# Kernel tuning notes

Hardware: AMD Instinct MI355X
Metric: run time of the kernel (lower is better)

The kernel has to match this reference:

```python
import jax, jax.numpy as jnp
from jax import lax
import numpy as np

B, M, C, H, W = 32, 2, 256, 16, 16
N = H * W            # 256, square case required by the original bmm chain
DIM = 256            # hardcoded self.dim in the module
THR = 0.1
RATIO = 0.8


def conv2d(x, w, b):
    y = lax.conv_general_dilated(x, w, (1, 1), 'SAME',
                                 dimension_numbers=('NCHW', 'OIHW', 'NCHW'))
    return y + b[None, :, None, None]


def setup_inputs() -> dict:
    key = jax.random.key(0)
    ks = jax.random.split(key, 8)
    return {
        'con_feat': jax.random.normal(ks[0], (B, M, C, H, W), jnp.float32),
        'feat_s':   jax.random.normal(ks[1], (B, M, C, C), jnp.float32),
        'feat_v':   jax.random.uniform(ks[2], (B, M, C), jnp.float32),
        'feat_d':   jax.random.normal(ks[3], (B, M, N, N), jnp.float32),
        'w_enc':    jax.random.normal(ks[4], (C, C, 3, 3), jnp.float32) * 0.02,
        'b_enc':    jnp.zeros((C,), jnp.float32),
        'w_dec':    jax.random.normal(ks[5], (C, C, 3, 3), jnp.float32) * 0.02,
        'b_dec':    jnp.zeros((C,), jnp.float32),
        'w_val':    jax.random.normal(ks[6], (1, 2 * C, 3, 3), jnp.float32) * 0.02,
        'b_val':    jnp.zeros((1,), jnp.float32),
    }


def _assemble(fs, fv, fd, counts):
    # fs: (M,C,C) row blocks, fv: (M,C) diag values, fd: (M,N,N) col blocks, counts: (M,)
    big = max(C, N)                                  # out-of-range sentinel -> dropped
    off = jnp.cumsum(counts) - counts                # exclusive prefix offsets (M,)
    r = jnp.arange(C)
    dest = off[:, None] + r[None, :]                 # (M,C) destination slots
    valid = (r[None, :] < counts[:, None]) & (dest >= 0)
    dest = jnp.where(valid, dest, big).reshape(-1)   # (M*C,)
    ns = jnp.zeros((C, C), fs.dtype).at[dest].set(fs.reshape(M * C, C), mode='drop')
    fd_cols = fd[:, :, :C].transpose(0, 2, 1).reshape(M * C, N)  # source columns as rows
    ndT = jnp.zeros((N, N), fd.dtype).at[dest].set(fd_cols, mode='drop')
    nv = jnp.zeros((C, N), fv.dtype).at[dest, dest].set(fv.reshape(-1), mode='drop')
    return ns, nv, ndT.T


def reference(con_feat, feat_s, feat_v, feat_d, w_enc, b_enc, w_dec, b_dec, w_val, b_val):
    x = con_feat.reshape(B * M, C, H, W)
    # autoencoder reconstruction loss (training branch)
    mid = jax.nn.relu(conv2d(x, w_enc, b_enc))
    x_rec = conv2d(mid, w_dec, b_dec)
    auto_enc_loss = jnp.mean((x - x_rec) ** 2)

    # data-dependent rank budget per (batch, modality)
    counts = jnp.sum(feat_v > THR, axis=-1).astype(jnp.int32)      # (B,M)
    total = jnp.sum(counts, axis=-1)                               # (B,)
    kmin = min(C, N)
    adj = jnp.round(kmin * counts.astype(jnp.float32)
                    / jnp.maximum(total, 1)[:, None].astype(jnp.float32)).astype(jnp.int32)
    if M > 1:
        adj = adj.at[:, -1].set(DIM - jnp.sum(adj[:, :-1], axis=-1))
    counts = jnp.maximum(jnp.where((total > kmin)[:, None], adj, counts), 0)

    # scatter-assemble s/v/d and reconstruct
    ns, nv, nd = jax.vmap(_assemble)(feat_s, feat_v, feat_d, counts)
    rec = jnp.matmul(jnp.matmul(ns, nv), nd)                        # (B,C,N)
    rec = rec.reshape(B, C, H, W)
    rec = conv2d(rec, w_dec, b_dec)                                 # decoder
    rec = (rec - rec.min()) / (rec.max() - rec.min()) * 2.0 - 1.0

    # per-modality value scores, softmax over modality
    scores = jnp.stack([
        jax.nn.sigmoid(jax.nn.relu(conv2d(
            jnp.concatenate([rec, con_feat[:, m]], axis=1), w_val, b_val)))
        for m in range(M)
    ], axis=1)                                                      # (B,M,1,H,W)
    scores = jax.nn.softmax(scores, axis=1)
    fused = jnp.sum((1.0 - RATIO) * scores * con_feat, axis=1) + rec * RATIO
    return fused, auto_enc_loss
```

## Files before the change

### kernel.cpp

```cpp
#include <hip/hip_runtime.h>
#include <math.h>


typedef __attribute__((ext_vector_type(8))) short short8;
typedef __attribute__((ext_vector_type(4))) float f32x4;

__device__ __forceinline__ void gload_lds16(const void* g, void* l) {
  __builtin_amdgcn_global_load_lds(
      (const __attribute__((address_space(1))) void*)g,
      (__attribute__((address_space(3))) void*)l, 16, 0, 0);
}

__device__ __forceinline__ unsigned short f2bf(float f) {
  unsigned u = __float_as_uint(f);
  unsigned r = (u + 0x7FFFu + ((u >> 16) & 1u)) >> 16;
  return (unsigned short)r;
}

__device__ __forceinline__ unsigned mapf(float f) {
  unsigned u = __float_as_uint(f);
  return (u & 0x80000000u) ? ~u : (u | 0x80000000u);
}
__device__ __forceinline__ float unmapf(unsigned u) {
  unsigned v = (u & 0x80000000u) ? (u & 0x7fffffffu) : ~u;
  return __uint_as_float(v);
}

__global__ __launch_bounds__(256) void prep_k(
    const float* __restrict__ cf, const float* __restrict__ we,
    const float* __restrict__ wd, const float* __restrict__ fv,
    unsigned short* __restrict__ Xp, unsigned short* __restrict__ WrE,
    unsigned short* __restrict__ WrD, int* __restrict__ smr,
    float* __restrict__ vd, float4* __restrict__ sraw4,
    float* __restrict__ lacc, unsigned* __restrict__ mm) {
  const int bx = blockIdx.x, t = threadIdx.x;
  if (bx < 2048) {
    int xcdP = bx >> 8, r = bx & 255;
    int img = xcdP * 8 + (r >> 5), ch = r & 31;
    int p = t;
    int ic0 = ch * 8;
    const float* sp = cf + (size_t)img * 65536 + (size_t)ic0 * 256 + p;
    unsigned short h[8];
#pragma unroll
    for (int i = 0; i < 8; ++i) h[i] = f2bf(sp[i * 256]);
    int y = p >> 4, x = p & 15;
    uint4 u;
    u.x = h[0] | (h[1] << 16); u.y = h[2] | (h[3] << 16);
    u.z = h[4] | (h[5] << 16); u.w = h[6] | (h[7] << 16);
    *(uint4*)&Xp[(size_t)img * 82944 + (size_t)(y * 18 + x + 19) * 256 + ic0] = u;
  } else if (bx < 2624) {
    int idx = (bx - 2048) * 256 + t;
    int ch = idx & 31, rest = idx >> 5;
    int s = rest % 9, ocx = rest / 9;
    int oc = ocx & 255, cv = ocx >> 8;
    const float* w = cv ? wd : we;
    unsigned short* o = cv ? WrD : WrE;
    int ic0 = ch * 8;
    unsigned short h[8];
#pragma unroll
    for (int i = 0; i < 8; ++i) h[i] = f2bf(w[(size_t)oc * 2304 + (ic0 + i) * 9 + s]);
    uint4 u;
    u.x = h[0] | (h[1] << 16); u.y = h[2] | (h[3] << 16);
    u.z = h[4] | (h[5] << 16); u.w = h[6] | (h[7] << 16);
    *(uint4*)&o[(size_t)oc * 2304 + s * 256 + ic0] = u;
  } else if (bx < 2752) {
    int img = bx - 2624;
    uint4* base = (uint4*)Xp + (size_t)img * 10368;
    uint4 z; z.x = z.y = z.z = z.w = 0;
    for (int it = t; it < 2176; it += 256) {
      int px = it >> 5, c = it & 31;
      int y, x;
      if (px < 18)      { y = 0;  x = px; }
      else if (px < 36) { y = 17; x = px - 18; }
      else if (px < 52) { y = px - 35; x = 0; }
      else              { y = px - 51; x = 17; }
      base[(y * 18 + x) * 32 + c] = z;
    }
  } else if (bx < 2784) {
    const int b = bx - 2752;
    const float v0 = fv[(size_t)b * 512 + t];
    const float v1 = fv[(size_t)b * 512 + 256 + t];
    const unsigned long long bal0 = __ballot(v0 > 0.1f);
    const unsigned long long bal1 = __ballot(v1 > 0.1f);
    __shared__ int cnt0[4], cnt1[4], fc[2];
    const int wid = t >> 6, lane = t & 63;
    if (lane == 0) { cnt0[wid] = __popcll(bal0); cnt1[wid] = __popcll(bal1); }
    smr[b * 256 + t] = -1;
    vd[b * 256 + t] = 0.f;
    __syncthreads();
    if (t == 0) {
      int c0 = cnt0[0] + cnt0[1] + cnt0[2] + cnt0[3];
      int c1 = cnt1[0] + cnt1[1] + cnt1[2] + cnt1[3];
      int total = c0 + c1;
      int f0, f1;
      if (total > 256) {
        int a0 = (int)rintf(256.0f * (float)c0 / (float)total);
        f0 = a0; f1 = 256 - a0;
      } else { f0 = c0; f1 = c1; }
      fc[0] = max(f0, 0); fc[1] = max(f1, 0);
    }
    __syncthreads();
    const int c0 = fc[0], c1 = fc[1];
    if (t < c0) { smr[b * 256 + t] = t; vd[b * 256 + t] = v0; }
    if (t < c1) {
      int d = c0 + t;
      if (d < 256) { smr[b * 256 + d] = 256 + t; vd[b * 256 + d] = v1; }
    }
  } else {
    int z = bx - 2784;
    if (z < 24) {
      float4 zz; zz.x = zz.y = zz.z = zz.w = 0.f;
      sraw4[z * 256 + t] = zz;
    } else if (t == 0) {
      lacc[0] = 0.f; mm[0] = 0xFFFFFFFFu; mm[1] = 0u;
    }
  }
}

__global__ __launch_bounds__(256) void ansbmt_k(
    const float* __restrict__ fs, const float* __restrict__ fd,
    const int* __restrict__ smr, const float* __restrict__ vd,
    unsigned short* __restrict__ Ans, unsigned short* __restrict__ BmT,
    unsigned short* __restrict__ Recp) {
  const int bx = blockIdx.x, t = threadIdx.x;
  if (bx < 1024) {
    int idx = bx * 256 + t;
    int ch = idx & 31, c = (idx >> 5) & 255, b = idx >> 13;
    int j0 = ch * 8;
    int si = smr[b * 256 + c];
    unsigned short h[8] = {0, 0, 0, 0, 0, 0, 0, 0};
    if (si >= 0) {
      int m = si >> 8, r = si & 255;
      const float* fp = fs + (((size_t)b * 2 + m) * 256 + r) * 256 + j0;
      const float* vp = vd + b * 256 + j0;
#pragma unroll
      for (int i = 0; i < 8; ++i) h[i] = f2bf(fp[i] * vp[i]);
    }
    uint4 u;
    u.x = h[0] | (h[1] << 16); u.y = h[2] | (h[3] << 16);
    u.z = h[4] | (h[5] << 16); u.w = h[6] | (h[7] << 16);
    *(uint4*)&Ans[(size_t)b * 65536 + c * 256 + j0] = u;
  } else if (bx < 2048) {
    __shared__ float sIn[4096];
    const int q0 = bx - 1024;
    const int b = q0 >> 5, jg = q0 & 31;
    const int sp = smr[b * 256 + t];
    const int m_p = sp >> 8, r_p = sp & 255;
#pragma unroll
    for (int u = 0; u < 4; ++u) {
      int q = t * 4 + u;
      int rr = q >> 6, w = q & 63;
      int m = rr >> 3, i = rr & 7;
      float4 f = ((const float4*)fd)[((size_t)(b * 2 + m) * 256 + jg * 8 + i) * 64 + w];
      *(float4*)&sIn[i * 512 + m * 256 + w * 4] = f;
    }
    __syncthreads();
    unsigned short h[8] = {0, 0, 0, 0, 0, 0, 0, 0};
    if (sp >= 0) {
#pragma unroll
      for (int i = 0; i < 8; ++i) h[i] = f2bf(sIn[i * 512 + m_p * 256 + r_p]);
    }
    uint4 u;
    u.x = h[0] | (h[1] << 16); u.y = h[2] | (h[3] << 16);
    u.z = h[4] | (h[5] << 16); u.w = h[6] | (h[7] << 16);
    *(uint4*)&BmT[(size_t)b * 65536 + t * 256 + jg * 8] = u;
  } else {
    int img = bx - 2048;
    uint4* base = (uint4*)Recp + (size_t)img * 10368;
    uint4 z; z.x = z.y = z.z = z.w = 0;
    for (int it = t; it < 2176; it += 256) {
      int px = it >> 5, c = it & 31;
      int y, x;
      if (px < 18)      { y = 0;  x = px; }
      else if (px < 36) { y = 17; x = px - 18; }
      else if (px < 52) { y = px - 35; x = 0; }
      else              { y = px - 51; x = 17; }
      base[(y * 18 + x) * 32 + c] = z;
    }
  }
}

__global__ __launch_bounds__(256, 3) void encrec_k(
    const unsigned short* __restrict__ Xin, const unsigned short* __restrict__ Wr,
    const float* __restrict__ bias,          unsigned short* __restrict__ outp,
    const unsigned short* __restrict__ BmT,  const unsigned short* __restrict__ Ans,
    unsigned short* __restrict__ Recp) {
  __shared__ __align__(16) char SS[49152];
  const int t = threadIdx.x, lane = t & 63, wave = t >> 6;
  const int L = blockIdx.x;

  if (L < 512) {
    char (*S)[24576] = (char(*)[24576])SS;
    const int xcd = L & 7, sl = L >> 3;
    const int img = xcd * 8 + (sl & 7);
    const int tile = sl >> 3;
    const int pt = tile & 3, ot = tile >> 2;

    int laneA[2], laneB[4];
#pragma unroll
    for (int r = 0; r < 2; ++r) {
      int id = r * 256 + t;
      int row = id >> 3, sub = id & 7, q = sub ^ (row & 7);
      int p = pt * 64 + row, y = p >> 4, x = p & 15;
      laneA[r] = (y * 18 + x) * 512 + q * 16;
    }
#pragma unroll
    for (int r = 0; r < 4; ++r) {
      int id = r * 256 + t;
      int row = id >> 3, sub = id & 7, q = sub ^ (row & 7);
      laneB[r] = (ot * 128 + row) * 4608 + q * 16;
    }
    const char* Ag = (const char*)Xin + (size_t)img * 165888;
    const char* Bg = (const char*)Wr;

    const int mlane = lane & 15, quad = lane >> 4;
    const int mw = wave >> 1, nw = wave & 1;
    int aoff[2][2], boff[4][2];
#pragma unroll
    for (int ks = 0; ks < 2; ++ks) {
#pragma unroll
      for (int i = 0; i < 2; ++i) {
        int rowm = mw * 32 + i * 16 + mlane;
        aoff[i][ks] = rowm * 128 + (((ks * 4 + quad) ^ (rowm & 7)) * 16);
      }
#pragma unroll
      for (int n = 0; n < 4; ++n) {
        int rown = nw * 64 + n * 16 + mlane;
        boff[n][ks] = 8192 + rown * 128 + (((ks * 4 + quad) ^ (rown & 7)) * 16);
      }
    }

    auto stage = [&](int kit, int buf) {
      int s = kit >> 2;
      int dy = s / 3, dx = s - dy * 3;
      int aG = (dy * 18 + dx) * 512 + (kit & 3) * 128;
      int bG = kit * 128;
      char* dst = S[buf];
#pragma unroll
      for (int r = 0; r < 2; ++r)
        gload_lds16(Ag + laneA[r] + aG, dst + r * 4096 + wave * 1024);
#pragma unroll
      for (int r = 0; r < 4; ++r)
        gload_lds16(Bg + laneB[r] + bG, dst + 8192 + r * 4096 + wave * 1024);
    };

    f32x4 acc[2][4] = {};
    auto compute = [&](int buf) {
      const char* Sb = S[buf];
#pragma unroll
      for (int ks = 0; ks < 2; ++ks) {
        short8 af[2], bf[4];
#pragma unroll
        for (int i = 0; i < 2; ++i) af[i] = *(const short8*)(Sb + aoff[i][ks]);
#pragma unroll
        for (int n = 0; n < 4; ++n) bf[n] = *(const short8*)(Sb + boff[n][ks]);
#pragma unroll
        for (int i = 0; i < 2; ++i)
#pragma unroll
          for (int n = 0; n < 4; ++n)
            acc[i][n] = __builtin_amdgcn_mfma_f32_16x16x32_bf16(af[i], bf[n], acc[i][n], 0, 0, 0);
      }
    };

    stage(0, 0);
    for (int kit = 0; kit < 36; ++kit) {
      int cur = kit & 1;
      asm volatile("s_waitcnt vmcnt(0)" ::: "memory");
      asm volatile("s_barrier" ::: "memory");
      if (kit + 1 < 36) stage(kit + 1, 1 - cur);
      compute(cur);
    }

#pragma unroll
    for (int i = 0; i < 2; ++i) {
      int m0 = pt * 64 + mw * 32 + i * 16 + quad * 4;
#pragma unroll
      for (int n = 0; n < 4; ++n) {
        int oc = ot * 128 + nw * 64 + n * 16 + mlane;
        float bv = bias[oc];
#pragma unroll
        for (int r = 0; r < 4; ++r) {
          int p = m0 + r;
          int y = p >> 4, x = p & 15;
          float v = fmaxf(acc[i][n][r] + bv, 0.f);
          outp[(size_t)img * 82944 + (size_t)(y * 18 + x + 19) * 256 + oc] = f2bf(v);
        }
      }
    }
  } else {
    unsigned short (*S)[8192] = (unsigned short(*)[8192])SS;
    const int L2 = L - 512;
    const int b = L2 >> 4, tile = L2 & 15;
    const int pt = tile >> 2, ct = tile & 3;

    int laneA[2], laneB[2];
#pragma unroll
    for (int j = 0; j < 2; ++j) {
      int id = (wave * 2 + j) * 64 + lane;
      int row = id >> 3, q = (id & 7) ^ (row & 7);
      laneA[j] = (pt * 64 + row) * 512 + q * 16;
      laneB[j] = (ct * 64 + row) * 512 + q * 16;
    }
    const char* Ag = (const char*)BmT + (size_t)b * 131072;
    const char* Bg = (const char*)Ans + (size_t)b * 131072;

    const int mlane = lane & 15, quad = lane >> 4;
    const int mw = wave >> 1, nw = wave & 1;
    int aoff[2][2], boff[2][2];
#pragma unroll
    for (int ks = 0; ks < 2; ++ks) {
#pragma unroll
      for (int i = 0; i < 2; ++i) {
        int rowm = mw * 32 + i * 16 + mlane;
        aoff[i][ks] = rowm * 128 + (((ks * 4 + quad) ^ (rowm & 7)) * 16);
        int rown = nw * 32 + i * 16 + mlane;
        boff[i][ks] = 8192 + rown * 128 + (((ks * 4 + quad) ^ (rown & 7)) * 16);
      }
    }

    auto stage = [&](int kit, int buf) {
      int g = kit * 128;
      char* dst = (char*)S[buf];
#pragma unroll
      for (int j = 0; j < 2; ++j)
        gload_lds16(Ag + laneA[j] + g, dst + (wave * 2 + j) * 1024);
#pragma unroll
      for (int j = 0; j < 2; ++j)
        gload_lds16(Bg + laneB[j] + g, dst + 8192 + (wave * 2 + j) * 1024);
    };

    f32x4 acc[2][2] = {};
    auto compute = [&](int buf) {
      const char* Sb = (const char*)S[buf];
#pragma unroll
      for (int ks = 0; ks < 2; ++ks) {
        short8 af[2], bf[2];
#pragma unroll
        for (int i = 0; i < 2; ++i) {
          af[i] = *(const short8*)(Sb + aoff[i][ks]);
          bf[i] = *(const short8*)(Sb + boff[i][ks]);
        }
#pragma unroll
        for (int i = 0; i < 2; ++i)
#pragma unroll
          for (int n = 0; n < 2; ++n)
            acc[i][n] = __builtin_amdgcn_mfma_f32_16x16x32_bf16(af[i], bf[n], acc[i][n], 0, 0, 0);
      }
    };

    stage(0, 0);
    stage(1, 1);
    for (int kit = 0; kit < 3; ++kit) {
      asm volatile("s_waitcnt vmcnt(4)" ::: "memory");
      asm volatile("s_barrier" ::: "memory");
      int nb = kit + 2;
      if (nb < 4) stage(nb, nb % 3);
      compute(kit % 3);
    }
    asm volatile("s_waitcnt vmcnt(0)" ::: "memory");
    asm volatile("s_barrier" ::: "memory");
    compute(3 % 3);

#pragma unroll
    for (int i = 0; i < 2; ++i) {
      int m0 = pt * 64 + mw * 32 + i * 16 + quad * 4;
#pragma unroll
      for (int n = 0; n < 2; ++n) {
        int cc = ct * 64 + nw * 32 + n * 16 + mlane;
#pragma unroll
        for (int r = 0; r < 4; ++r) {
          int p = m0 + r;
          int y = p >> 4, x = p & 15;
          Recp[(size_t)b * 82944 + (size_t)(y * 18 + x + 19) * 256 + cc] = f2bf(acc[i][n][r]);
        }
      }
    }
  }
}

__global__ __launch_bounds__(256, 3) void conv_dec_k(
    const unsigned short* __restrict__ Midp, const unsigned short* __restrict__ Recp,
    const unsigned short* __restrict__ Wr, const float* __restrict__ bias,
    const float* __restrict__ cfref, float* __restrict__ rec2,
    float* __restrict__ lacc, unsigned* __restrict__ mm) {
  __shared__ __align__(16) char S[2][24576];
  const int t = threadIdx.x, lane = t & 63, wave = t >> 6;
  const int L = blockIdx.x;
  const int xcd = L & 7, sl = L >> 3;
  const int u12 = sl % 12, tile = sl / 12;
  const bool isLoss = u12 < 8;
  const int unit = isLoss ? (xcd * 8 + u12) : (64 + xcd * 4 + (u12 - 8));
  const int pt = tile & 3, ot = tile >> 2;

  int laneA[2], laneB[4];
#pragma unroll
  for (int r = 0; r < 2; ++r) {
    int id = r * 256 + t;
    int row = id >> 3, sub = id & 7, q = sub ^ (row & 7);
    int p = pt * 64 + row, y = p >> 4, x = p & 15;
    laneA[r] = (y * 18 + x) * 512 + q * 16;
  }
#pragma unroll
  for (int r = 0; r < 4; ++r) {
    int id = r * 256 + t;
    int row = id >> 3, sub = id & 7, q = sub ^ (row & 7);
    laneB[r] = (ot * 128 + row) * 4608 + q * 16;
  }
  const char* Ag = isLoss ? (const char*)Midp + (size_t)unit * 165888
                          : (const char*)Recp + (size_t)(unit - 64) * 165888;
  const char* Bg = (const char*)Wr;

  const int mlane = lane & 15, quad = lane >> 4;
  const int mw = wave >> 1, nw = wave & 1;
  int aoff[2][2], boff[4][2];
#pragma unroll
  for (int ks = 0; ks < 2; ++ks) {
#pragma unroll
    for (int i = 0; i < 2; ++i) {
      int rowm = mw * 32 + i * 16 + mlane;
      aoff[i][ks] = rowm * 128 + (((ks * 4 + quad) ^ (rowm & 7)) * 16);
    }
#pragma unroll
    for (int n = 0; n < 4; ++n) {
      int rown = nw * 64 + n * 16 + mlane;
      boff[n][ks] = 8192 + rown * 128 + (((ks * 4 + quad) ^ (rown & 7)) * 16);
    }
  }

  auto stage = [&](int kit, int buf) {
    int s = kit >> 2;
    int dy = s / 3, dx = s - dy * 3;
    int aG = (dy * 18 + dx) * 512 + (kit & 3) * 128;
    int bG = kit * 128;
    char* dst = S[buf];
#pragma unroll
    for (int r = 0; r < 2; ++r)
      gload_lds16(Ag + laneA[r] + aG, dst + r * 4096 + wave * 1024);
#pragma unroll
    for (int r = 0; r < 4; ++r)
      gload_lds16(Bg + laneB[r] + bG, dst + 8192 + r * 4096 + wave * 1024);
  };

  f32x4 acc[2][4] = {};
  auto compute = [&](int buf) {
    const char* Sb = S[buf];
#pragma unroll
    for (int ks = 0; ks < 2; ++ks) {
      short8 af[2], bf[4];
#pragma unroll
      for (int i = 0; i < 2; ++i) af[i] = *(const short8*)(Sb + aoff[i][ks]);
#pragma unroll
      for (int n = 0; n < 4; ++n) bf[n] = *(const short8*)(Sb + boff[n][ks]);
#pragma unroll
      for (int i = 0; i < 2; ++i)
#pragma unroll
        for (int n = 0; n < 4; ++n)
          acc[i][n] = __builtin_amdgcn_mfma_f32_16x16x32_bf16(af[i], bf[n], acc[i][n], 0, 0, 0);
    }
  };

  stage(0, 0);
  for (int kit = 0; kit < 36; ++kit) {
    int cur = kit & 1;
    asm volatile("s_waitcnt vmcnt(0)" ::: "memory");
    asm volatile("s_barrier" ::: "memory");
    if (kit + 1 < 36) stage(kit + 1, 1 - cur);
    compute(cur);
  }

  if (isLoss) {
    float ls = 0.f;
#pragma unroll
    for (int i = 0; i < 2; ++i) {
      int m0 = pt * 64 + mw * 32 + i * 16 + quad * 4;
#pragma unroll
      for (int n = 0; n < 4; ++n) {
        int oc = ot * 128 + nw * 64 + n * 16 + mlane;
        float bv = bias[oc];
        float4 c4 = *(const float4*)(cfref + (size_t)unit * 65536 + (size_t)oc * 256 + m0);
        float d0 = acc[i][n][0] + bv - c4.x;
        float d1 = acc[i][n][1] + bv - c4.y;
        float d2 = acc[i][n][2] + bv - c4.z;
        float d3 = acc[i][n][3] + bv - c4.w;
        ls += d0 * d0 + d1 * d1 + d2 * d2 + d3 * d3;
      }
    }
#pragma unroll
    for (int off = 32; off; off >>= 1) ls += __shfl_down(ls, off);
    __shared__ float sred[4];
    if (lane == 0) sred[wave] = ls;
    __syncthreads();
    if (t == 0) {
      float s = sred[0] + sred[1] + sred[2] + sred[3];
      atomicAdd(lacc, s);
    }
  } else {
    const int img2 = unit - 64;
    float mn = INFINITY, mx = -INFINITY;
#pragma unroll
    for (int i = 0; i < 2; ++i) {
      int m0 = pt * 64 + mw * 32 + i * 16 + quad * 4;
#pragma unroll
      for (int n = 0; n < 4; ++n) {
        int oc = ot * 128 + nw * 64 + n * 16 + mlane;
        float bv = bias[oc];
        float4 v;
        v.x = acc[i][n][0] + bv; v.y = acc[i][n][1] + bv;
        v.z = acc[i][n][2] + bv; v.w = acc[i][n][3] + bv;
        mn = fminf(mn, fminf(fminf(v.x, v.y), fminf(v.z, v.w)));
        mx = fmaxf(mx, fmaxf(fmaxf(v.x, v.y), fmaxf(v.z, v.w)));
        *(float4*)(rec2 + (size_t)img2 * 65536 + (size_t)oc * 256 + m0) = v;
      }
    }
#pragma unroll
    for (int off = 32; off; off >>= 1) {
      mn = fminf(mn, __shfl_down(mn, off));
      mx = fmaxf(mx, __shfl_down(mx, off));
    }
    __shared__ float smn[4], smx[4];
    if (lane == 0) { smn[wave] = mn; smx[wave] = mx; }
    __syncthreads();
    if (t == 0) {
      float a = fminf(fminf(smn[0], smn[1]), fminf(smn[2], smn[3]));
      float b2 = fmaxf(fmaxf(smx[0], smx[1]), fmaxf(smx[2], smx[3]));
      atomicMin(&mm[0], mapf(a));
      atomicMax(&mm[1], mapf(b2));
    }
  }
}

__global__ __launch_bounds__(256) void score_conv_k(
    const float* __restrict__ rec2, const float* __restrict__ cf,
    const float* __restrict__ wval, const unsigned* __restrict__ mm,
    float* __restrict__ sraw) {
  const int b = blockIdx.x, phase = blockIdx.y, icc = blockIdx.z;
  const int t = threadIdx.x;
  const int row = t >> 4, col = t & 15;
  __shared__ float s_in[8 * 360];
  __shared__ float s_wv[72];
  for (int i = t; i < 8 * 360; i += 256) s_in[i] = 0.f;
  const float* src;
  float sc = 1.f, sh = 0.f;
  int wofs;
  if (phase == 0) {
    src = rec2 + (size_t)b * 65536;
    float mn = unmapf(mm[0]), mx = unmapf(mm[1]);
    sc = 2.f / (mx - mn);
    sh = -mn * sc - 1.f;
    wofs = 0;
  } else {
    src = cf + ((size_t)b * 2 + (phase - 1)) * 65536;
    wofs = 2304;
  }
  float acc = 0.f;
  for (int ic0 = icc * 32; ic0 < icc * 32 + 32; ic0 += 8) {
    __syncthreads();
#pragma unroll
    for (int i = 0; i < 8; ++i) {
      float v = src[(ic0 + i) * 256 + t];
      if (phase == 0) v = fmaf(v, sc, sh);
      s_in[i * 360 + (row + 1) * 20 + (col + 1)] = v;
    }
    if (t < 72) s_wv[t] = wval[wofs + ic0 * 9 + t];
    __syncthreads();
#pragma unroll
    for (int i = 0; i < 8; ++i)
#pragma unroll
      for (int ky = 0; ky < 3; ++ky)
#pragma unroll
        for (int kx = 0; kx < 3; ++kx)
          acc += s_in[i * 360 + (row + ky) * 20 + (col + kx)] * s_wv[i * 9 + ky * 3 + kx];
  }
  atomicAdd(&sraw[((size_t)b * 3 + phase) * 256 + t], acc);
}

__global__ __launch_bounds__(256) void fuse_k(
    const float* __restrict__ cf, const float* __restrict__ rec2,
    const float* __restrict__ sraw, const float* __restrict__ bval,
    const unsigned* __restrict__ mm, const float* __restrict__ lacc,
    float* __restrict__ outp) {
  const int e0 = (blockIdx.x * 256 + threadIdx.x) * 4;
  const int b = e0 >> 16;
  const int rest = e0 & 65535;
  const int pos = e0 & 255;
  const float mn = unmapf(mm[0]), mx = unmapf(mm[1]);
  const float sc = 2.f / (mx - mn), sh = -mn * sc - 1.f;
  const float4 srec = *(const float4*)&sraw[(size_t)b * 768 + pos];
  const float4 scA  = *(const float4*)&sraw[(size_t)b * 768 + 256 + pos];
  const float4 scB  = *(const float4*)&sraw[(size_t)b * 768 + 512 + pos];
  const float bv = bval[0];
  const float4 r4 = *(const float4*)&rec2[e0];
  const float4 f0 = *(const float4*)&cf[(size_t)b * 131072 + rest];
  const float4 f1 = *(const float4*)&cf[(size_t)b * 131072 + 65536 + rest];
  float4 o;
#pragma unroll
  for (int k = 0; k < 4; ++k) {
    float sr = ((const float*)&srec)[k];
    float a0 = ((const float*)&scA)[k];
    float a1 = ((const float*)&scB)[k];
    float z0 = fmaxf(sr + a0 + bv, 0.f);
    float z1 = fmaxf(sr + a1 + bv, 0.f);
    float s0 = 1.f / (1.f + expf(-z0));
    float s1 = 1.f / (1.f + expf(-z1));
    float w0 = 1.f / (1.f + expf(s1 - s0));
    float w1 = 1.f - w0;
    float rn = fmaf(((const float*)&r4)[k], sc, sh);
    float g0 = ((const float*)&f0)[k];
    float g1 = ((const float*)&f1)[k];
    ((float*)&o)[k] = 0.2f * (w0 * g0 + w1 * g1) + 0.8f * rn;
  }
  *(float4*)&outp[e0] = o;
  if (e0 == 0) outp[2097152] = lacc[0] * (1.f / 4194304.f);
}

extern "C" void kernel_launch(void* const* d_in, const int* in_sizes, int n_in,
                              void* d_out, int out_size, void* d_ws, size_t ws_size,
                              hipStream_t stream) {
  const float* cf    = (const float*)d_in[0];
  const float* fs    = (const float*)d_in[1];
  const float* fv    = (const float*)d_in[2];
  const float* fd    = (const float*)d_in[3];
  const float* w_enc = (const float*)d_in[4];
  const float* b_enc = (const float*)d_in[5];
  const float* w_dec = (const float*)d_in[6];
  const float* b_dec = (const float*)d_in[7];
  const float* w_val = (const float*)d_in[8];
  const float* b_val = (const float*)d_in[9];
  float* out = (float*)d_out;
  float* wsf = (float*)d_ws;

  unsigned short* Xp   = (unsigned short*)wsf;
  unsigned short* Midp = (unsigned short*)(wsf + 2654208);
  unsigned short* Recp = (unsigned short*)(wsf + 5308416);
  float* rec2 = wsf + 6635520;
  unsigned short* WrE = (unsigned short*)(wsf + 8732672);
  unsigned short* WrD = (unsigned short*)(wsf + 9027584);
  unsigned short* Ans = (unsigned short*)(wsf + 9322496);
  unsigned short* BmT = (unsigned short*)(wsf + 10371072);
  float* sraw = wsf + 11419648;
  float* vd   = wsf + 11444224;
  int*   smr  = (int*)(wsf + 11452416);
  float* lacc = wsf + 11460608;
  unsigned* mm = (unsigned*)(wsf + 11460609);

  prep_k<<<2809, 256, 0, stream>>>(cf, w_enc, w_dec, fv, Xp, WrE, WrD, smr, vd,
                                   (float4*)sraw, lacc, mm);
  ansbmt_k<<<2080, 256, 0, stream>>>(fs, fd, smr, vd, Ans, BmT, Recp);
  encrec_k<<<1024, 256, 0, stream>>>(Xp, WrE, b_enc, Midp, BmT, Ans, Recp);
  conv_dec_k<<<768, 256, 0, stream>>>(Midp, Recp, WrD, b_dec, cf, rec2, lacc, mm);
  score_conv_k<<<dim3(32, 3, 8), 256, 0, stream>>>(rec2, cf, w_val, mm, sraw);
  fuse_k<<<2048, 256, 0, stream>>>(cf, rec2, sraw, b_val, mm, lacc, out);
}
```

Before: 212.5 us.

## Merge prep and assemble kernels; store decoder output as bf16

Folds the ansbmt kernel into the prep kernel. Each assemble block now recomputes the per-batch modality counts from feat_v with ballots instead of reading smr/vd index tables, which removes one launch and the dependency between them. The decoder output rec2 is stored as bf16 rather than fp32, halving its write and the two later reads in score_conv and fuse. Score_conv also reads weights directly from global memory instead of staging them in LDS. The cost is redundant count computation per block and reduced precision on the reconstruction used in the output.

Measured after the change: 219.9 us. +3.5%, slower.

```diff
diff --git a/kernel.cpp b/kernel.cpp
--- a/kernel.cpp
+++ b/kernel.cpp
@@ -16,6 +16,9 @@
   unsigned r = (u + 0x7FFFu + ((u >> 16) & 1u)) >> 16;
   return (unsigned short)r;
 }
+__device__ __forceinline__ float bf2f(unsigned short h) {
+  return __uint_as_float(((unsigned)h) << 16);
+}
 
 __device__ __forceinline__ unsigned mapf(float f) {
   unsigned u = __float_as_uint(f);
@@ -26,13 +29,15 @@
   return __uint_as_float(v);
 }
 
-__global__ __launch_bounds__(256) void prep_k(
+__global__ __launch_bounds__(256) void prep2_k(
     const float* __restrict__ cf, const float* __restrict__ we,
     const float* __restrict__ wd, const float* __restrict__ fv,
+    const float* __restrict__ fs, const float* __restrict__ fd,
     unsigned short* __restrict__ Xp, unsigned short* __restrict__ WrE,
-    unsigned short* __restrict__ WrD, int* __restrict__ smr,
-    float* __restrict__ vd, float4* __restrict__ sraw4,
-    float* __restrict__ lacc, unsigned* __restrict__ mm) {
+    unsigned short* __restrict__ WrD, unsigned short* __restrict__ Ans,
+    unsigned short* __restrict__ BmT, unsigned short* __restrict__ Recp,
+    float4* __restrict__ sraw4, float* __restrict__ lacc,
+    unsigned* __restrict__ mm) {
   const int bx = blockIdx.x, t = threadIdx.x;
   if (bx < 2048) {
     int xcdP = bx >> 8, r = bx & 255;
@@ -76,75 +81,65 @@
       else              { y = px - 51; x = 17; }
       base[(y * 18 + x) * 32 + c] = z;
     }
-  } else if (bx < 2784) {
-    const int b = bx - 2752;
+  } else if (bx < 3776) {
+    const int abx = bx - 2752;
+    const int b = abx >> 5;
     const float v0 = fv[(size_t)b * 512 + t];
     const float v1 = fv[(size_t)b * 512 + 256 + t];
     const unsigned long long bal0 = __ballot(v0 > 0.1f);
     const unsigned long long bal1 = __ballot(v1 > 0.1f);
-    __shared__ int cnt0[4], cnt1[4], fc[2];
-    const int wid = t >> 6, lane = t & 63;
-    if (lane == 0) { cnt0[wid] = __popcll(bal0); cnt1[wid] = __popcll(bal1); }
-    smr[b * 256 + t] = -1;
-    vd[b * 256 + t] = 0.f;
+    __shared__ int c0a[4], c1a[4];
+    if ((t & 63) == 0) { c0a[t >> 6] = __popcll(bal0); c1a[t >> 6] = __popcll(bal1); }
     __syncthreads();
-    if (t == 0) {
-      int c0 = cnt0[0] + cnt0[1] + cnt0[2] + cnt0[3];
-      int c1 = cnt1[0] + cnt1[1] + cnt1[2] + cnt1[3];
-      int total = c0 + c1;
-      int f0, f1;
-      if (total > 256) {
-        int a0 = (int)rintf(256.0f * (float)c0 / (float)total);
-        f0 = a0; f1 = 256 - a0;
-      } else { f0 = c0; f1 = c1; }
-      fc[0] = max(f0, 0); fc[1] = max(f1, 0);
-    }
-    __syncthreads();
-    const int c0 = fc[0], c1 = fc[1];
-    if (t < c0) { smr[b * 256 + t] = t; vd[b * 256 + t] = v0; }
-    if (t < c1) {
-      int d = c0 + t;
-      if (d < 256) { smr[b * 256 + d] = 256 + t; vd[b * 256 + d] = v1; }
-    }
-  } else {
-    int z = bx - 2784;
-    if (z < 24) {
-      float4 zz; zz.x = zz.y = zz.z = zz.w = 0.f;
-      sraw4[z * 256 + t] = zz;
-    } else if (t == 0) {
-      lacc[0] = 0.f; mm[0] = 0xFFFFFFFFu; mm[1] = 0u;
-    }
-  }
-}
-
-__global__ __launch_bounds__(256) void ansbmt_k(
-    const float* __restrict__ fs, const float* __restrict__ fd,
-    const int* __restrict__ smr, const float* __restrict__ vd,
-    unsigned short* __restrict__ Ans, unsigned short* __restrict__ BmT,
-    unsigned short* __restrict__ Recp) {
-  const int bx = blockIdx.x, t = threadIdx.x;
-  if (bx < 1024) {
-    int idx = bx * 256 + t;
-    int ch = idx & 31, c = (idx >> 5) & 255, b = idx >> 13;
+    int c0 = c0a[0] + c0a[1] + c0a[2] + c0a[3];
+    int c1 = c1a[0] + c1a[1] + c1a[2] + c1a[3];
+    int total = c0 + c1, f0, f1;
+    if (total > 256) {
+      int a0 = (int)rintf(256.0f * (float)c0 / (float)total);
+      f0 = a0; f1 = 256 - a0;
+    } else { f0 = c0; f1 = c1; }
+    f0 = max(f0, 0); f1 = max(f1, 0);
+
+    int idx = abx * 256 + t;
+    int ch = idx & 31, c = (idx >> 5) & 255;
     int j0 = ch * 8;
-    int si = smr[b * 256 + c];
+    int si = (c < f0) ? c : ((c < f0 + f1) ? (256 + (c - f0)) : -1);
     unsigned short h[8] = {0, 0, 0, 0, 0, 0, 0, 0};
     if (si >= 0) {
       int m = si >> 8, r = si & 255;
       const float* fp = fs + (((size_t)b * 2 + m) * 256 + r) * 256 + j0;
-      const float* vp = vd + b * 256 + j0;
-#pragma unroll
-      for (int i = 0; i < 8; ++i) h[i] = f2bf(fp[i] * vp[i]);
+#pragma unroll
+      for (int i = 0; i < 8; ++i) {
+        int j = j0 + i;
+        float vdj = (j < f0) ? fv[(size_t)b * 512 + j]
+                  : ((j < f0 + f1) ? fv[(size_t)b * 512 + 256 + (j - f0)] : 0.f);
+        h[i] = f2bf(fp[i] * vdj);
+      }
     }
     uint4 u;
     u.x = h[0] | (h[1] << 16); u.y = h[2] | (h[3] << 16);
     u.z = h[4] | (h[5] << 16); u.w = h[6] | (h[7] << 16);
     *(uint4*)&Ans[(size_t)b * 65536 + c * 256 + j0] = u;
-  } else if (bx < 2048) {
+  } else if (bx < 4800) {
     __shared__ float sIn[4096];
-    const int q0 = bx - 1024;
+    const int q0 = bx - 3776;
     const int b = q0 >> 5, jg = q0 & 31;
-    const int sp = smr[b * 256 + t];
+    const float v0 = fv[(size_t)b * 512 + t];
+    const float v1 = fv[(size_t)b * 512 + 256 + t];
+    const unsigned long long bal0 = __ballot(v0 > 0.1f);
+    const unsigned long long bal1 = __ballot(v1 > 0.1f);
+    __shared__ int c0a[4], c1a[4];
+    if ((t & 63) == 0) { c0a[t >> 6] = __popcll(bal0); c1a[t >> 6] = __popcll(bal1); }
+    __syncthreads();
+    int c0 = c0a[0] + c0a[1] + c0a[2] + c0a[3];
+    int c1 = c1a[0] + c1a[1] + c1a[2] + c1a[3];
+    int total = c0 + c1, f0, f1;
+    if (total > 256) {
+      int a0 = (int)rintf(256.0f * (float)c0 / (float)total);
+      f0 = a0; f1 = 256 - a0;
+    } else { f0 = c0; f1 = c1; }
+    f0 = max(f0, 0); f1 = max(f1, 0);
+    const int sp = (t < f0) ? t : ((t < f0 + f1) ? (256 + (t - f0)) : -1);
     const int m_p = sp >> 8, r_p = sp & 255;
 #pragma unroll
     for (int u = 0; u < 4; ++u) {
@@ -164,8 +159,8 @@
     u.x = h[0] | (h[1] << 16); u.y = h[2] | (h[3] << 16);
     u.z = h[4] | (h[5] << 16); u.w = h[6] | (h[7] << 16);
     *(uint4*)&BmT[(size_t)b * 65536 + t * 256 + jg * 8] = u;
-  } else {
-    int img = bx - 2048;
+  } else if (bx < 4832) {
+    int img = bx - 4800;
     uint4* base = (uint4*)Recp + (size_t)img * 10368;
     uint4 z; z.x = z.y = z.z = z.w = 0;
     for (int it = t; it < 2176; it += 256) {
@@ -177,6 +172,14 @@
       else              { y = px - 51; x = 17; }
       base[(y * 18 + x) * 32 + c] = z;
     }
+  } else {
+    int z = bx - 4832;
+    if (z < 24) {
+      float4 zz; zz.x = zz.y = zz.z = zz.w = 0.f;
+      sraw4[z * 256 + t] = zz;
+    } else if (t == 0) {
+      lacc[0] = 0.f; mm[0] = 0xFFFFFFFFu; mm[1] = 0u;
+    }
   }
 }
 
@@ -381,7 +384,7 @@
 __global__ __launch_bounds__(256, 3) void conv_dec_k(
     const unsigned short* __restrict__ Midp, const unsigned short* __restrict__ Recp,
     const unsigned short* __restrict__ Wr, const float* __restrict__ bias,
-    const float* __restrict__ cfref, float* __restrict__ rec2,
+    const float* __restrict__ cfref, unsigned short* __restrict__ rec2b,
     float* __restrict__ lacc, unsigned* __restrict__ mm) {
   __shared__ __align__(16) char S[2][24576];
   const int t = threadIdx.x, lane = t & 63, wave = t >> 6;
@@ -504,12 +507,13 @@
       for (int n = 0; n < 4; ++n) {
         int oc = ot * 128 + nw * 64 + n * 16 + mlane;
         float bv = bias[oc];
-        float4 v;
-        v.x = acc[i][n][0] + bv; v.y = acc[i][n][1] + bv;
-        v.z = acc[i][n][2] + bv; v.w = acc[i][n][3] + bv;
-        mn = fminf(mn, fminf(fminf(v.x, v.y), fminf(v.z, v.w)));
-        mx = fmaxf(mx, fmaxf(fmaxf(v.x, v.y), fmaxf(v.z, v.w)));
-        *(float4*)(rec2 + (size_t)img2 * 65536 + (size_t)oc * 256 + m0) = v;
+        float v0 = acc[i][n][0] + bv, v1 = acc[i][n][1] + bv;
+        float v2 = acc[i][n][2] + bv, v3 = acc[i][n][3] + bv;
+        mn = fminf(mn, fminf(fminf(v0, v1), fminf(v2, v3)));
+        mx = fmaxf(mx, fmaxf(fmaxf(v0, v1), fmaxf(v2, v3)));
+        ushort4 hq;
+        hq.x = f2bf(v0); hq.y = f2bf(v1); hq.z = f2bf(v2); hq.w = f2bf(v3);
+        *(ushort4*)(rec2b + (size_t)img2 * 65536 + (size_t)oc * 256 + m0) = hq;
       }
     }
 #pragma unroll
@@ -530,26 +534,24 @@
 }
 
 __global__ __launch_bounds__(256) void score_conv_k(
-    const float* __restrict__ rec2, const float* __restrict__ cf,
+    const unsigned short* __restrict__ rec2b, const float* __restrict__ cf,
     const float* __restrict__ wval, const unsigned* __restrict__ mm,
     float* __restrict__ sraw) {
   const int b = blockIdx.x, phase = blockIdx.y, icc = blockIdx.z;
   const int t = threadIdx.x;
   const int row = t >> 4, col = t & 15;
   __shared__ float s_in[8 * 360];
-  __shared__ float s_wv[72];
   for (int i = t; i < 8 * 360; i += 256) s_in[i] = 0.f;
-  const float* src;
   float sc = 1.f, sh = 0.f;
   int wofs;
+  const float* srcf = nullptr;
   if (phase == 0) {
-    src = rec2 + (size_t)b * 65536;
     float mn = unmapf(mm[0]), mx = unmapf(mm[1]);
     sc = 2.f / (mx - mn);
     sh = -mn * sc - 1.f;
     wofs = 0;
   } else {
-    src = cf + ((size_t)b * 2 + (phase - 1)) * 65536;
+    srcf = cf + ((size_t)b * 2 + (phase - 1)) * 65536;
     wofs = 2304;
   }
   float acc = 0.f;
@@ -557,11 +559,13 @@
     __syncthreads();
 #pragma unroll
     for (int i = 0; i < 8; ++i) {
-      float v = src[(ic0 + i) * 256 + t];
-      if (phase == 0) v = fmaf(v, sc, sh);
+      float v;
+      if (phase == 0)
+        v = fmaf(bf2f(rec2b[(size_t)b * 65536 + (ic0 + i) * 256 + t]), sc, sh);
+      else
+        v = srcf[(ic0 + i) * 256 + t];
       s_in[i * 360 + (row + 1) * 20 + (col + 1)] = v;
     }
-    if (t < 72) s_wv[t] = wval[wofs + ic0 * 9 + t];
     __syncthreads();
 #pragma unroll
     for (int i = 0; i < 8; ++i)
@@ -569,13 +573,14 @@
       for (int ky = 0; ky < 3; ++ky)
 #pragma unroll
         for (int kx = 0; kx < 3; ++kx)
-          acc += s_in[i * 360 + (row + ky) * 20 + (col + kx)] * s_wv[i * 9 + ky * 3 + kx];
+          acc += s_in[i * 360 + (row + ky) * 20 + (col + kx)] *
+                 wval[wofs + (ic0 + i) * 9 + ky * 3 + kx];
   }
   atomicAdd(&sraw[((size_t)b * 3 + phase) * 256 + t], acc);
 }
 
 __global__ __launch_bounds__(256) void fuse_k(
-    const float* __restrict__ cf, const float* __restrict__ rec2,
+    const float* __restrict__ cf, const unsigned short* __restrict__ rec2b,
     const float* __restrict__ sraw, const float* __restrict__ bval,
     const unsigned* __restrict__ mm, const float* __restrict__ lacc,
     float* __restrict__ outp) {
@@ -589,9 +594,10 @@
   const float4 scA  = *(const float4*)&sraw[(size_t)b * 768 + 256 + pos];
   const float4 scB  = *(const float4*)&sraw[(size_t)b * 768 + 512 + pos];
   const float bv = bval[0];
-  const float4 r4 = *(const float4*)&rec2[e0];
+  const ushort4 rh = *(const ushort4*)&rec2b[e0];
   const float4 f0 = *(const float4*)&cf[(size_t)b * 131072 + rest];
   const float4 f1 = *(const float4*)&cf[(size_t)b * 131072 + 65536 + rest];
+  float rn4[4] = {bf2f(rh.x), bf2f(rh.y), bf2f(rh.z), bf2f(rh.w)};
   float4 o;
 #pragma unroll
   for (int k = 0; k < 4; ++k) {
@@ -604,7 +610,7 @@
     float s1 = 1.f / (1.f + expf(-z1));
     float w0 = 1.f / (1.f + expf(s1 - s0));
     float w1 = 1.f - w0;
-    float rn = fmaf(((const float*)&r4)[k], sc, sh);
+    float rn = fmaf(rn4[k], sc, sh);
     float g0 = ((const float*)&f0)[k];
     float g1 = ((const float*)&f1)[k];
     ((float*)&o)[k] = 0.2f * (w0 * g0 + w1 * g1) + 0.8f * rn;
@@ -632,22 +638,19 @@
   unsigned short* Xp   = (unsigned short*)wsf;
   unsigned short* Midp = (unsigned short*)(wsf + 2654208);
   unsigned short* Recp = (unsigned short*)(wsf + 5308416);
-  float* rec2 = wsf + 6635520;
+  unsigned short* rec2b = (unsigned short*)(wsf + 6635520);
   unsigned short* WrE = (unsigned short*)(wsf + 8732672);
   unsigned short* WrD = (unsigned short*)(wsf + 9027584);
   unsigned short* Ans = (unsigned short*)(wsf + 9322496);
   unsigned short* BmT = (unsigned short*)(wsf + 10371072);
   float* sraw = wsf + 11419648;
-  float* vd   = wsf + 11444224;
-  int*   smr  = (int*)(wsf + 11452416);
   float* lacc = wsf + 11460608;
   unsigned* mm = (unsigned*)(wsf + 11460609);
 
-  prep_k<<<2809, 256, 0, stream>>>(cf, w_enc, w_dec, fv, Xp, WrE, WrD, smr, vd,
-                                   (float4*)sraw, lacc, mm);
-  ansbmt_k<<<2080, 256, 0, stream>>>(fs, fd, smr, vd, Ans, BmT, Recp);
+  prep2_k<<<4857, 256, 0, stream>>>(cf, w_enc, w_dec, fv, fs, fd, Xp, WrE, WrD,
+                                    Ans, BmT, Recp, (float4*)sraw, lacc, mm);
   encrec_k<<<1024, 256, 0, stream>>>(Xp, WrE, b_enc, Midp, BmT, Ans, Recp);
-  conv_dec_k<<<768, 256, 0, stream>>>(Midp, Recp, WrD, b_dec, cf, rec2, lacc, mm);
-  score_conv_k<<<dim3(32, 3, 8), 256, 0, stream>>>(rec2, cf, w_val, mm, sraw);
-  fuse_k<<<2048, 256, 0, stream>>>(cf, rec2, sraw, b_val, mm, lacc, out);
-}
+  conv_dec_k<<<768, 256, 0, stream>>>(Midp, Recp, WrD, b_dec, cf, rec2b, lacc, mm);
+  score_conv_k<<<dim3(32, 3, 8), 256, 0, stream>>>(rec2b, cf, w_val, mm, sraw);
+  fuse_k<<<2048, 256, 0, stream>>>(cf, rec2b, sraw, b_val, mm, lacc, out);
+}
```

## Move con_feat score convolutions into encrec kernel to overlap with GEMMs

Applied to the files above, without the earlier changes.

The score convolution over the con_feat half of the value-conv input does not depend on the reconstruction, so those blocks (phases 1 and 2) now run as extra blocks appended to encrec_k's grid. score_conv_k keeps only the reconstruction phase, which shrinks its grid to a third. The aim is to hide that work inside an earlier, heavier launch and shorten the critical tail. The cost is that encrec_k gets more blocks that compete with the MFMA blocks for CUs and LDS.

Result: no change. 212.8 us (+0.1%).

```diff
diff --git a/kernel.cpp b/kernel.cpp
--- a/kernel.cpp
+++ b/kernel.cpp
@@ -184,7 +184,8 @@
     const unsigned short* __restrict__ Xin, const unsigned short* __restrict__ Wr,
     const float* __restrict__ bias,          unsigned short* __restrict__ outp,
     const unsigned short* __restrict__ BmT,  const unsigned short* __restrict__ Ans,
-    unsigned short* __restrict__ Recp) {
+    unsigned short* __restrict__ Recp,       const float* __restrict__ cf,
+    const float* __restrict__ wval,          float* __restrict__ sraw) {
   __shared__ __align__(16) char SS[49152];
   const int t = threadIdx.x, lane = t & 63, wave = t >> 6;
   const int L = blockIdx.x;
@@ -287,7 +288,7 @@
         }
       }
     }
-  } else {
+  } else if (L < 1024) {
     unsigned short (*S)[8192] = (unsigned short(*)[8192])SS;
     const int L2 = L - 512;
     const int b = L2 >> 4, tile = L2 & 15;
@@ -375,6 +376,32 @@
         }
       }
     }
+  } else {
+    const int u = L - 1024;
+    const int b = u & 31, phase = 1 + ((u >> 5) & 1), icc = u >> 6;
+    const int row = t >> 4, col = t & 15;
+    float* s_in = (float*)SS;
+    float* s_wv = (float*)(SS + 11776);
+    for (int i = t; i < 8 * 360; i += 256) s_in[i] = 0.f;
+    const float* srcf = cf + ((size_t)b * 2 + (phase - 1)) * 65536;
+    const int wofs = 2304;
+    float acc = 0.f;
+    for (int ic0 = icc * 32; ic0 < icc * 32 + 32; ic0 += 8) {
+      __syncthreads();
+#pragma unroll
+      for (int i = 0; i < 8; ++i)
+        s_in[i * 360 + (row + 1) * 20 + (col + 1)] = srcf[(ic0 + i) * 256 + t];
+      if (t < 72) s_wv[t] = wval[wofs + ic0 * 9 + t];
+      __syncthreads();
+#pragma unroll
+      for (int i = 0; i < 8; ++i)
+#pragma unroll
+        for (int ky = 0; ky < 3; ++ky)
+#pragma unroll
+          for (int kx = 0; kx < 3; ++kx)
+            acc += s_in[i * 360 + (row + ky) * 20 + (col + kx)] * s_wv[i * 9 + ky * 3 + kx];
+    }
+    atomicAdd(&sraw[((size_t)b * 3 + phase) * 256 + t], acc);
   }
 }
 
@@ -530,38 +557,27 @@
 }
 
 __global__ __launch_bounds__(256) void score_conv_k(
-    const float* __restrict__ rec2, const float* __restrict__ cf,
-    const float* __restrict__ wval, const unsigned* __restrict__ mm,
-    float* __restrict__ sraw) {
-  const int b = blockIdx.x, phase = blockIdx.y, icc = blockIdx.z;
+    const float* __restrict__ rec2, const float* __restrict__ wval,
+    const unsigned* __restrict__ mm, float* __restrict__ sraw) {
+  const int b = blockIdx.x, icc = blockIdx.z;
   const int t = threadIdx.x;
   const int row = t >> 4, col = t & 15;
   __shared__ float s_in[8 * 360];
   __shared__ float s_wv[72];
   for (int i = t; i < 8 * 360; i += 256) s_in[i] = 0.f;
-  const float* src;
-  float sc = 1.f, sh = 0.f;
-  int wofs;
-  if (phase == 0) {
-    src = rec2 + (size_t)b * 65536;
-    float mn = unmapf(mm[0]), mx = unmapf(mm[1]);
-    sc = 2.f / (mx - mn);
-    sh = -mn * sc - 1.f;
-    wofs = 0;
-  } else {
-    src = cf + ((size_t)b * 2 + (phase - 1)) * 65536;
-    wofs = 2304;
-  }
+  const float* src = rec2 + (size_t)b * 65536;
+  float mn = unmapf(mm[0]), mx = unmapf(mm[1]);
+  float sc = 2.f / (mx - mn);
+  float sh = -mn * sc - 1.f;
   float acc = 0.f;
   for (int ic0 = icc * 32; ic0 < icc * 32 + 32; ic0 += 8) {
     __syncthreads();
 #pragma unroll
     for (int i = 0; i < 8; ++i) {
-      float v = src[(ic0 + i) * 256 + t];
-      if (phase == 0) v = fmaf(v, sc, sh);
+      float v = fmaf(src[(ic0 + i) * 256 + t], sc, sh);
       s_in[i * 360 + (row + 1) * 20 + (col + 1)] = v;
     }
-    if (t < 72) s_wv[t] = wval[wofs + ic0 * 9 + t];
+    if (t < 72) s_wv[t] = wval[ic0 * 9 + t];
     __syncthreads();
 #pragma unroll
     for (int i = 0; i < 8; ++i)
@@ -571,7 +587,7 @@
         for (int kx = 0; kx < 3; ++kx)
           acc += s_in[i * 360 + (row + ky) * 20 + (col + kx)] * s_wv[i * 9 + ky * 3 + kx];
   }
-  atomicAdd(&sraw[((size_t)b * 3 + phase) * 256 + t], acc);
+  atomicAdd(&sraw[(size_t)b * 768 + t], acc);
 }
 
 __global__ __launch_bounds__(256) void fuse_k(
@@ -646,8 +662,9 @@
   prep_k<<<2809, 256, 0, stream>>>(cf, w_enc, w_dec, fv, Xp, WrE, WrD, smr, vd,
                                    (float4*)sraw, lacc, mm);
   ansbmt_k<<<2080, 256, 0, stream>>>(fs, fd, smr, vd, Ans, BmT, Recp);
-  encrec_k<<<1024, 256, 0, stream>>>(Xp, WrE, b_enc, Midp, BmT, Ans, Recp);
+  encrec_k<<<1536, 256, 0, stream>>>(Xp, WrE, b_enc, Midp, BmT, Ans, Recp,
+                                     cf, w_val, sraw);
   conv_dec_k<<<768, 256, 0, stream>>>(Midp, Recp, WrD, b_dec, cf, rec2, lacc, mm);
-  score_conv_k<<<dim3(32, 3, 8), 256, 0, stream>>>(rec2, cf, w_val, mm, sraw);
+  score_conv_k<<<dim3(32, 1, 8), 256, 0, stream>>>(rec2, w_val, mm, sraw);
   fuse_k<<<2048, 256, 0, stream>>>(cf, rec2, sraw, b_val, mm, lacc, out);
 }
```
